# Kernel optimization log

Measured on AMD Instinct MI355X. Metric: run time of the kernel, lower is better.

## Reference

```python
import jax, jax.numpy as jnp
import numpy as np


def setup_inputs() -> dict:
    key = jax.random.key(0)
    ks = jax.random.split(key, 12)
    N, F, H, E = 100000, 128, 128, 625000
    x = jax.random.normal(ks[0], (N, F), dtype=jnp.float32)
    edge_index = jax.random.randint(ks[1], (2, E), 0, N, dtype=jnp.int64)
    s1 = 1.0 / np.sqrt(2 * F)
    s2 = 1.0 / np.sqrt(H)
    W1 = jax.random.uniform(ks[2], (2 * F, H), jnp.float32, -s1, s1)
    b1 = jax.random.uniform(ks[3], (H,), jnp.float32, -s1, s1)
    W2 = jax.random.uniform(ks[4], (H, H), jnp.float32, -s2, s2)
    b2 = jax.random.uniform(ks[5], (H,), jnp.float32, -s2, s2)
    W3 = jax.random.uniform(ks[6], (H, H), jnp.float32, -s2, s2)
    b3 = jax.random.uniform(ks[7], (H,), jnp.float32, -s2, s2)
    W4 = jax.random.uniform(ks[8], (H, 1), jnp.float32, -s2, s2)
    b4 = jax.random.uniform(ks[9], (1,), jnp.float32, -s2, s2)
    return {"x": x, "edge_index": edge_index, "W1": W1, "b1": b1,
            "W2": W2, "b2": b2, "W3": W3, "b3": b3, "W4": W4, "b4": b4}


def reference(x, edge_index, W1, b1, W2, b2, W3, b3, W4, b4):
    # Gather endpoint features and concat -> [E, 2F]
    x_i = x[edge_index[0], :]
    x_j = x[edge_index[1], :]
    ef = jnp.concatenate([x_i, x_j], axis=-1)
    h = jax.nn.relu(ef @ W1 + b1)
    h = jax.nn.relu(h @ W2 + b2)
    h = jax.nn.relu(h @ W3 + b3)
    return jax.nn.sigmoid(h @ W4 + b4)  # [E, 1]
```

## Files before the change

kernel.cpp:

```cpp
#include <hip/hip_runtime.h>
#include <math.h>

typedef _Float16 half8 __attribute__((ext_vector_type(8)));
typedef _Float16 half2v __attribute__((ext_vector_type(2)));
typedef float f32x4 __attribute__((ext_vector_type(4)));
typedef float f32x16 __attribute__((ext_vector_type(16)));

#define HDIM 128
#define WHALFS 65536
#define SCR_HALFS 2048
#define LDS_HALFS (WHALFS + 8 * SCR_HALFS)
#define LDS_BYTES (LDS_HALFS * 2)

__device__ __forceinline__ void gld_lds16(const _Float16* g, _Float16* l)
{
    __builtin_amdgcn_global_load_lds(
        (const __attribute__((address_space(1))) void*)g,
        (__attribute__((address_space(3))) void*)l, 16, 0, 0);
}

__global__ __launch_bounds__(256) void prep_kernel(
    const float* __restrict__ x,  const float* __restrict__ W1,
    const float* __restrict__ W2, const float* __restrict__ W3,
    _Float16* __restrict__ xh,  _Float16* __restrict__ W1p,
    _Float16* __restrict__ W2p, _Float16* __restrict__ W3p, int NF)
{
    int bid = blockIdx.x;
    if (bid < 32) {
        int t = bid * 256 + threadIdx.x;
        const float* W; _Float16* Wp; int KS; int u;
        if (t < 4096)      { W = W1; Wp = W1p; KS = 16; u = t; }
        else if (t < 6144) { W = W2; Wp = W2p; KS = 8;  u = t - 4096; }
        else               { W = W3; Wp = W3p; KS = 8;  u = t - 6144; }
        int lane = u & 63;
        int fk   = u >> 6;
        int ks   = fk % KS;
        int mt   = fk / KS;
        int m    = mt * 32 + (lane & 31);
        int k0   = ks * 16 + (lane >> 5) * 8;
        half8 v;
        #pragma unroll
        for (int j = 0; j < 8; ++j) v[j] = (_Float16)W[(k0 + j) * HDIM + m];
        *(half8*)(Wp + (size_t)u * 8) = v;
    } else {
        const long stride = (long)(gridDim.x - 32) * 256;
        for (long u = (long)(bid - 32) * 256 + threadIdx.x; u * 8 < (long)NF; u += stride) {
            long i = u * 8;
            const float4* xf = (const float4*)(x + i);
            float4 f0 = xf[0], f1 = xf[1];
            half8 v;
            v[0] = (_Float16)f0.x; v[1] = (_Float16)f0.y;
            v[2] = (_Float16)f0.z; v[3] = (_Float16)f0.w;
            v[4] = (_Float16)f1.x; v[5] = (_Float16)f1.y;
            v[6] = (_Float16)f1.z; v[7] = (_Float16)f1.w;
            *(half8*)(xh + i) = v;
        }
    }
}

__device__ __forceinline__ void acc_bias_init(
    f32x16 (&acc)[4], const float* __restrict__ bias, int H)
{
    #pragma unroll
    for (int mt = 0; mt < 4; ++mt)
        #pragma unroll
        for (int g = 0; g < 4; ++g) {
            float4 bv = *(const float4*)(bias + mt * 32 + g * 8 + H * 4);
            acc[mt][4 * g + 0] = bv.x;
            acc[mt][4 * g + 1] = bv.y;
            acc[mt][4 * g + 2] = bv.z;
            acc[mt][4 * g + 3] = bv.w;
        }
}

__device__ __forceinline__ void epi_exchange(
    f32x16 (&acc)[4], half8 (&bh)[8], int H)
{
    #pragma unroll
    for (int mt = 0; mt < 4; ++mt) {
        unsigned w[8], pw[8];
        #pragma unroll
        for (int g = 0; g < 8; ++g) {
            union { half2v v; unsigned u; } cv;
            cv.v[0] = (_Float16)fmaxf(acc[mt][2 * g],     0.f);
            cv.v[1] = (_Float16)fmaxf(acc[mt][2 * g + 1], 0.f);
            w[g] = cv.u;
        }
        #pragma unroll
        for (int g = 0; g < 8; ++g)
            pw[g] = (unsigned)__shfl_xor((int)w[g], 32, 64);
        union { unsigned u[4]; half8 h; } f0, f1;
        f0.u[0] = H ? pw[2] : w[0];
        f0.u[1] = H ? pw[3] : w[1];
        f0.u[2] = H ? w[2]  : pw[0];
        f0.u[3] = H ? w[3]  : pw[1];
        f1.u[0] = H ? pw[6] : w[4];
        f1.u[1] = H ? pw[7] : w[5];
        f1.u[2] = H ? w[6]  : pw[4];
        f1.u[3] = H ? w[7]  : pw[5];
        bh[2 * mt]     = f0.h;
        bh[2 * mt + 1] = f1.h;
    }
}

__device__ __forceinline__ void layer_mfma(
    f32x16 (&acc)[4], const _Float16* __restrict__ Wl,
    half8 (&bh)[8], int lane)
{
    __builtin_amdgcn_s_setprio(1);
    #pragma unroll
    for (int ks = 0; ks < 8; ++ks) {
        half8 aw[4];
        #pragma unroll
        for (int mt = 0; mt < 4; ++mt)
            aw[mt] = *(const half8*)(Wl + ((size_t)((mt * 8 + ks) * 64 + lane)) * 8);
        #pragma unroll
        for (int mt = 0; mt < 4; ++mt)
            acc[mt] = __builtin_amdgcn_mfma_f32_32x32x16_f16(
                aw[mt], bh[ks], acc[mt], 0, 0, 0);
    }
    __builtin_amdgcn_s_setprio(0);
}

__device__ __forceinline__ void l1_chunk(
    f32x16 (&acc)[4], const _Float16* __restrict__ W1l,
    half8 (&bef)[4], int ks0, int lane)
{
    __builtin_amdgcn_s_setprio(1);
    #pragma unroll
    for (int ks = 0; ks < 4; ++ks) {
        half8 aw[4];
        #pragma unroll
        for (int mt = 0; mt < 4; ++mt)
            aw[mt] = *(const half8*)(W1l + ((size_t)((mt * 16 + ks0 + ks) * 64 + lane)) * 8);
        #pragma unroll
        for (int mt = 0; mt < 4; ++mt)
            acc[mt] = __builtin_amdgcn_mfma_f32_32x32x16_f16(
                aw[mt], bef[ks], acc[mt], 0, 0, 0);
    }
    __builtin_amdgcn_s_setprio(0);
}

__global__ __launch_bounds__(512, 2) void edge_mlp_kernel(
    const int* __restrict__ ei, const _Float16* __restrict__ xh,
    const _Float16* __restrict__ wpack,
    const float* __restrict__ b1, const float* __restrict__ b2,
    const float* __restrict__ b3, const float* __restrict__ W4,
    const float* __restrict__ b4, float* __restrict__ out, int E)
{
    extern __shared__ _Float16 lds[];

    {
        float4* dst = (float4*)lds;
        const float4* src = (const float4*)wpack;
        #pragma unroll
        for (int i = 0; i < 16; ++i)
            dst[i * 512 + threadIdx.x] = src[i * 512 + threadIdx.x];
    }
    __syncthreads();

    const int tid  = threadIdx.x;
    const int wave = tid >> 6;
    const int lane = tid & 63;
    const int e32  = lane & 31;
    const int H    = lane >> 5;

    const _Float16* W1l = lds;
    const _Float16* W2l = lds + 32768;
    const _Float16* W3l = lds + 49152;
    _Float16* scr = lds + WHALFS + wave * SCR_HALFS;

    const int ntiles = (E + 255) >> 8;
    const float b4v = b4[0];

    int gi, gj;
    {
        const int row = min(blockIdx.x * 256 + wave * 32 + e32, E - 1);
        gi = ei[row];
        gj = ei[E + row];
    }

    for (int t = blockIdx.x; t < ntiles; t += gridDim.x) {
        const int base = t * 256 + wave * 32;

        {
            const _Float16* pj = xh + (size_t)gj * HDIM + 64 + H * 8;
            #pragma unroll
            for (int c = 0; c < 4; ++c)
                gld_lds16(pj + c * 16, scr + c * 512);
        }

        half8 bef[4];
        {
            const _Float16* pi = xh + (size_t)gi * HDIM + H * 8;
            #pragma unroll
            for (int c = 0; c < 4; ++c)
                bef[c] = *(const half8*)(pi + c * 16);
        }

        f32x16 acc[4];
        acc_bias_init(acc, b1, H);

        half8 befB[4];
        {
            const _Float16* pi = xh + (size_t)gi * HDIM + 64 + H * 8;
            #pragma unroll
            for (int c = 0; c < 4; ++c)
                befB[c] = *(const half8*)(pi + c * 16);
        }
        l1_chunk(acc, W1l, bef, 0, lane);

        {
            const _Float16* pj = xh + (size_t)gj * HDIM + H * 8;
            #pragma unroll
            for (int c = 0; c < 4; ++c)
                bef[c] = *(const half8*)(pj + c * 16);
        }
        l1_chunk(acc, W1l, befB, 4, lane);

        l1_chunk(acc, W1l, bef, 8, lane);

        asm volatile("s_waitcnt vmcnt(0)" ::: "memory");
        __builtin_amdgcn_s_setprio(1);
        #pragma unroll
        for (int c = 0; c < 4; ++c) {
            half8 bj = *(const half8*)(scr + c * 512 + lane * 8);
            half8 aw[4];
            #pragma unroll
            for (int mt = 0; mt < 4; ++mt)
                aw[mt] = *(const half8*)(W1l + ((size_t)((mt * 16 + 12 + c) * 64 + lane)) * 8);
            #pragma unroll
            for (int mt = 0; mt < 4; ++mt)
                acc[mt] = __builtin_amdgcn_mfma_f32_32x32x16_f16(
                    aw[mt], bj, acc[mt], 0, 0, 0);
        }
        __builtin_amdgcn_s_setprio(0);

        half8 bh[8];
        epi_exchange(acc, bh, H);
        acc_bias_init(acc, b2, H);

        int gin, gjn;
        {
            const int rown = min(min(t + (int)gridDim.x, ntiles - 1) * 256
                                 + wave * 32 + e32, E - 1);
            gin = ei[rown];
            gjn = ei[E + rown];
        }

        layer_mfma(acc, W2l, bh, lane);
        epi_exchange(acc, bh, H);
        acc_bias_init(acc, b3, H);
        layer_mfma(acc, W3l, bh, lane);

        {
            float s = 0.f;
            #pragma unroll
            for (int mt = 0; mt < 4; ++mt)
                #pragma unroll
                for (int g = 0; g < 4; ++g) {
                    float4 w4v = *(const float4*)(W4 + mt * 32 + g * 8 + H * 4);
                    s += fmaxf(acc[mt][4 * g + 0], 0.f) * w4v.x;
                    s += fmaxf(acc[mt][4 * g + 1], 0.f) * w4v.y;
                    s += fmaxf(acc[mt][4 * g + 2], 0.f) * w4v.z;
                    s += fmaxf(acc[mt][4 * g + 3], 0.f) * w4v.w;
                }
            s += __shfl_xor(s, 32, 64);
            const int row = base + e32;
            if (lane < 32 && row < E)
                out[row] = 1.f / (1.f + __expf(-(s + b4v)));
        }

        gi = gin; gj = gjn;
    }
}

extern "C" void kernel_launch(void* const* d_in, const int* in_sizes, int n_in,
                              void* d_out, int out_size, void* d_ws, size_t ws_size,
                              hipStream_t stream)
{
    const float* x  = (const float*)d_in[0];
    const int*   ei = (const int*)d_in[1];
    const float* W1 = (const float*)d_in[2];
    const float* b1 = (const float*)d_in[3];
    const float* W2 = (const float*)d_in[4];
    const float* b2 = (const float*)d_in[5];
    const float* W3 = (const float*)d_in[6];
    const float* b3 = (const float*)d_in[7];
    const float* W4 = (const float*)d_in[8];
    const float* b4 = (const float*)d_in[9];
    float* out = (float*)d_out;

    const int NF = 100000 * 128;
    const int E  = out_size;

    _Float16* xh  = (_Float16*)d_ws;
    _Float16* W1p = xh + NF;
    _Float16* W2p = W1p + 32768;
    _Float16* W3p = W2p + 16384;

    prep_kernel<<<32 + 2048, 256, 0, stream>>>(x, W1, W2, W3, xh, W1p, W2p, W3p, NF);

    hipFuncSetAttribute((const void*)edge_mlp_kernel,
                        hipFuncAttributeMaxDynamicSharedMemorySize, LDS_BYTES);
    edge_mlp_kernel<<<256, 512, LDS_BYTES, stream>>>(ei, xh, W1p,
                                                     b1, b2, b3, W4, b4, out, E);
}
```

Before: 203.6 us.

## Drop LDS scratch staging and grow blocks to twelve waves

Removes the per-wave LDS scratch buffer that staged the last quarter of the j-node features via global_load_lds, and loads them into registers instead, reusing the befB buffer. With the LDS footprint cut to just the weights, each block grows from 8 to 12 waves, tiles grow from 256 to 384 edges, and launch bounds become 768 threads. The aim is more waves per CU to hide gather latency. The launch bound tightens the per-thread register budget, which may cause spills, and the async LDS load path is lost.

Measured after the change: 353.5 us. 1.74x slower.

```diff
diff --git a/kernel.cpp b/kernel.cpp
--- a/kernel.cpp
+++ b/kernel.cpp
@@ -8,16 +8,7 @@
 
 #define HDIM 128
 #define WHALFS 65536
-#define SCR_HALFS 2048
-#define LDS_HALFS (WHALFS + 8 * SCR_HALFS)
-#define LDS_BYTES (LDS_HALFS * 2)
-
-__device__ __forceinline__ void gld_lds16(const _Float16* g, _Float16* l)
-{
-    __builtin_amdgcn_global_load_lds(
-        (const __attribute__((address_space(1))) void*)g,
-        (__attribute__((address_space(3))) void*)l, 16, 0, 0);
-}
+#define LDS_BYTES (WHALFS * 2)
 
 __global__ __launch_bounds__(256) void prep_kernel(
     const float* __restrict__ x,  const float* __restrict__ W1,
@@ -141,7 +132,7 @@
     __builtin_amdgcn_s_setprio(0);
 }
 
-__global__ __launch_bounds__(512, 2) void edge_mlp_kernel(
+__global__ __launch_bounds__(768, 3) void edge_mlp_kernel(
     const int* __restrict__ ei, const _Float16* __restrict__ xh,
     const _Float16* __restrict__ wpack,
     const float* __restrict__ b1, const float* __restrict__ b2,
@@ -153,9 +144,8 @@
     {
         float4* dst = (float4*)lds;
         const float4* src = (const float4*)wpack;
-        #pragma unroll
-        for (int i = 0; i < 16; ++i)
-            dst[i * 512 + threadIdx.x] = src[i * 512 + threadIdx.x];
+        for (int i = threadIdx.x; i < 8192; i += 768)
+            dst[i] = src[i];
     }
     __syncthreads();
 
@@ -168,27 +158,19 @@
     const _Float16* W1l = lds;
     const _Float16* W2l = lds + 32768;
     const _Float16* W3l = lds + 49152;
-    _Float16* scr = lds + WHALFS + wave * SCR_HALFS;
-
-    const int ntiles = (E + 255) >> 8;
+
+    const int ntiles = (E + 383) / 384;
     const float b4v = b4[0];
 
     int gi, gj;
     {
-        const int row = min(blockIdx.x * 256 + wave * 32 + e32, E - 1);
+        const int row = min(blockIdx.x * 384 + wave * 32 + e32, E - 1);
         gi = ei[row];
         gj = ei[E + row];
     }
 
     for (int t = blockIdx.x; t < ntiles; t += gridDim.x) {
-        const int base = t * 256 + wave * 32;
-
-        {
-            const _Float16* pj = xh + (size_t)gj * HDIM + 64 + H * 8;
-            #pragma unroll
-            for (int c = 0; c < 4; ++c)
-                gld_lds16(pj + c * 16, scr + c * 512);
-        }
+        const int base = t * 384 + wave * 32;
 
         half8 bef[4];
         {
@@ -218,23 +200,15 @@
         }
         l1_chunk(acc, W1l, befB, 4, lane);
 
+        {
+            const _Float16* pj = xh + (size_t)gj * HDIM + 64 + H * 8;
+            #pragma unroll
+            for (int c = 0; c < 4; ++c)
+                befB[c] = *(const half8*)(pj + c * 16);
+        }
         l1_chunk(acc, W1l, bef, 8, lane);
 
-        asm volatile("s_waitcnt vmcnt(0)" ::: "memory");
-        __builtin_amdgcn_s_setprio(1);
-        #pragma unroll
-        for (int c = 0; c < 4; ++c) {
-            half8 bj = *(const half8*)(scr + c * 512 + lane * 8);
-            half8 aw[4];
-            #pragma unroll
-            for (int mt = 0; mt < 4; ++mt)
-                aw[mt] = *(const half8*)(W1l + ((size_t)((mt * 16 + 12 + c) * 64 + lane)) * 8);
-            #pragma unroll
-            for (int mt = 0; mt < 4; ++mt)
-                acc[mt] = __builtin_amdgcn_mfma_f32_32x32x16_f16(
-                    aw[mt], bj, acc[mt], 0, 0, 0);
-        }
-        __builtin_amdgcn_s_setprio(0);
+        l1_chunk(acc, W1l, befB, 12, lane);
 
         half8 bh[8];
         epi_exchange(acc, bh, H);
@@ -242,7 +216,7 @@
 
         int gin, gjn;
         {
-            const int rown = min(min(t + (int)gridDim.x, ntiles - 1) * 256
+            const int rown = min(min(t + (int)gridDim.x, ntiles - 1) * 384
                                  + wave * 32 + e32, E - 1);
             gin = ei[rown];
             gjn = ei[E + rown];
@@ -303,6 +277,6 @@
 
     hipFuncSetAttribute((const void*)edge_mlp_kernel,
                         hipFuncAttributeMaxDynamicSharedMemorySize, LDS_BYTES);
-    edge_mlp_kernel<<<256, 512, LDS_BYTES, stream>>>(ei, xh, W1p,
+    edge_mlp_kernel<<<256, 768, LDS_BYTES, stream>>>(ei, xh, W1p,
                                                      b1, b2, b3, W4, b4, out, E);
 }
```
